# Kernel optimization log

Hardware: AMD Instinct MI355X
Metric: run time of the kernel (lower is better)

The kernel has to match this reference:

```python
import jax, jax.numpy as jnp
import numpy as np

HID = 50

def _lstm_cell(x_t, h, c, W_ih, W_hh, b_ih, b_hh):
    # PyTorch LSTMCell gate order: i, f, g, o
    gates = x_t @ W_ih.T + b_ih + h @ W_hh.T + b_hh  # [B, 4*HID]
    i, f, g, o = jnp.split(gates, 4, axis=-1)
    i = jax.nn.sigmoid(i)
    f = jax.nn.sigmoid(f)
    g = jnp.tanh(g)
    o = jax.nn.sigmoid(o)
    c = f * c + i * g
    h = o * jnp.tanh(c)
    return h, c


def setup_inputs() -> dict:
    key = jax.random.key(0)
    ks = jax.random.split(key, 8)
    B, T = 2048, 512
    stdv = 1.0 / np.sqrt(HID)
    x = jax.random.normal(ks[0], (B, T), dtype=jnp.float32)
    W_ih = jax.random.uniform(ks[1], (4 * HID, 1), jnp.float32, -stdv, stdv)
    W_hh = jax.random.uniform(ks[2], (4 * HID, HID), jnp.float32, -stdv, stdv)
    b_ih = jax.random.uniform(ks[3], (4 * HID,), jnp.float32, -stdv, stdv)
    b_hh = jax.random.uniform(ks[4], (4 * HID,), jnp.float32, -stdv, stdv)
    W_out = jax.random.uniform(ks[5], (1, HID), jnp.float32, -stdv, stdv)
    b_out = jax.random.uniform(ks[6], (1,), jnp.float32, -stdv, stdv)
    return {"x": x, "W_ih": W_ih, "W_hh": W_hh, "b_ih": b_ih,
            "b_hh": b_hh, "W_out": W_out, "b_out": b_out, "future": 64}


def reference(x, W_ih, W_hh, b_ih, b_hh, W_out, b_out, future):
    B, T = x.shape
    h0 = jnp.zeros((B, HID), dtype=x.dtype)
    c0 = jnp.zeros((B, HID), dtype=x.dtype)
    xs = x.T[:, :, None]  # [T, B, 1]

    def seq_step(carry, x_t):
        h, c = carry
        h, c = _lstm_cell(x_t, h, c, W_ih, W_hh, b_ih, b_hh)
        out = h @ W_out.T + b_out  # [B, 1]
        return (h, c), out

    (h, c), outs = jax.lax.scan(seq_step, (h0, c0), xs)  # outs: [T, B, 1]

    def fut_step(carry, _):
        h, c, out = carry
        h, c = _lstm_cell(out, h, c, W_ih, W_hh, b_ih, b_hh)
        out = h @ W_out.T + b_out
        return (h, c, out), out

    _, fut_outs = jax.lax.scan(fut_step, (h, c, outs[-1]), None, length=future)
    all_outs = jnp.concatenate([outs, fut_outs], axis=0)  # [T+future, B, 1]
    return jnp.transpose(all_outs[:, :, 0])  # [B, T+future]
```

## Files before the change

kernel.cpp:

```cpp
#include <hip/hip_runtime.h>

typedef float v2f __attribute__((ext_vector_type(2)));
typedef float v4f __attribute__((ext_vector_type(4)));

#define BATCH 2048
#define TSEQ 512
#define FUT 64
#define TOUT (TSEQ + FUT)
#define HID 50
#define RPB 4

__device__ __forceinline__ float rcp_f(float x) { return __builtin_amdgcn_rcpf(x); }
__device__ __forceinline__ float sigm(float x)  { return rcp_f(1.f + __expf(-x)); }
__device__ __forceinline__ float tanh_f(float x){ return 1.f - 2.f * rcp_f(__expf(2.f * x) + 1.f); }

__device__ __forceinline__ void pkfma(v2f& acc, v2f a, v2f b) {
  asm("v_pk_fma_f32 %0, %1, %2, %0" : "+v"(acc) : "v"(a), "v"(b));
}

__global__ __launch_bounds__(256, 2) void lstm_seq_kernel(
    const float* __restrict__ x,
    const float* __restrict__ W_ih,
    const float* __restrict__ W_hh,
    const float* __restrict__ b_ih,
    const float* __restrict__ b_hh,
    const float* __restrict__ W_out,
    const float* __restrict__ b_out,
    float* __restrict__ out)
{
  __shared__ float sW[4 * HID * HID];
  __shared__ float sx[RPB][TSEQ];
  __shared__ float sH[RPB][64];

  const int tid  = threadIdx.x;
  const int wv   = tid >> 6;
  const int lane = tid & 63;
  const int row  = blockIdx.x * RPB + wv;

  for (int i = tid; i < 4 * HID * HID; i += 256) sW[i] = W_hh[i];
  for (int i = lane; i < TSEQ; i += 64) sx[wv][i] = x[row * TSEQ + i];
  sH[wv][lane] = 0.f;
  __syncthreads();

  const bool act = (lane < HID);
  const int  kk  = act ? lane : 0;

  v2f wi[25], wf[25], wg[25], wo[25];
  {
    const v2f* r0 = (const v2f*)&sW[(0 * HID + kk) * HID];
    const v2f* r1 = (const v2f*)&sW[(1 * HID + kk) * HID];
    const v2f* r2 = (const v2f*)&sW[(2 * HID + kk) * HID];
    const v2f* r3 = (const v2f*)&sW[(3 * HID + kk) * HID];
    #pragma unroll
    for (int j = 0; j < 25; ++j) { wi[j] = r0[j]; wf[j] = r1[j]; wg[j] = r2[j]; wo[j] = r3[j]; }
  }
  const float bi = b_ih[0 * HID + kk] + b_hh[0 * HID + kk];
  const float bf = b_ih[1 * HID + kk] + b_hh[1 * HID + kk];
  const float bg = b_ih[2 * HID + kk] + b_hh[2 * HID + kk];
  const float bo = b_ih[3 * HID + kk] + b_hh[3 * HID + kk];
  const float wxi = W_ih[0 * HID + kk];
  const float wxf = W_ih[1 * HID + kk];
  const float wxg = W_ih[2 * HID + kk];
  const float wxo = W_ih[3 * HID + kk];
  const float wout = act ? W_out[kk] : 0.f;
  const float bout = b_out[0];

  float h = 0.f, c = 0.f, oprev = 0.f;
  float* orow = out + (size_t)row * TOUT;
  const v4f* sH4 = (const v4f*)sH[wv];
  const v2f* sH2 = (const v2f*)sH[wv];

  auto step = [&](float xv, int t) {
    sH[wv][lane] = h;
    v2f ai2 = {fmaf(xv, wxi, bi), 0.f};
    v2f af2 = {fmaf(xv, wxf, bf), 0.f};
    v2f ag2 = {fmaf(xv, wxg, bg), 0.f};
    v2f ao2 = {fmaf(xv, wxo, bo), 0.f};
    #pragma unroll
    for (int q = 0; q < 12; ++q) {
      v4f h4 = sH4[q];
      v2f ha = {h4.x, h4.y}, hb = {h4.z, h4.w};
      pkfma(ai2, wi[2 * q], ha); pkfma(ai2, wi[2 * q + 1], hb);
      pkfma(af2, wf[2 * q], ha); pkfma(af2, wf[2 * q + 1], hb);
      pkfma(ag2, wg[2 * q], ha); pkfma(ag2, wg[2 * q + 1], hb);
      pkfma(ao2, wo[2 * q], ha); pkfma(ao2, wo[2 * q + 1], hb);
    }
    {
      v2f ht = sH2[24];
      pkfma(ai2, wi[24], ht); pkfma(af2, wf[24], ht);
      pkfma(ag2, wg[24], ht); pkfma(ao2, wo[24], ht);
    }
    float gi = sigm(ai2.x + ai2.y);
    float gf = sigm(af2.x + af2.y);
    float gg = tanh_f(ag2.x + ag2.y);
    float go = sigm(ao2.x + ao2.y);
    c = fmaf(gf, c, gi * gg);
    float hn = go * tanh_f(c);
    h = act ? hn : 0.f;
    float p = h * wout;
    p += __shfl_xor(p, 1);
    p += __shfl_xor(p, 2);
    p += __shfl_xor(p, 4);
    p += __shfl_xor(p, 8);
    p += __shfl_xor(p, 16);
    p += __shfl_xor(p, 32);
    float ot = p + bout;
    if (lane == 0) orow[t] = ot;
    oprev = ot;
  };

  #pragma unroll 1
  for (int t = 0; t < TSEQ; ++t) step(sx[wv][t], t);
  #pragma unroll 1
  for (int t = TSEQ; t < TOUT; ++t) step(oprev, t);
}

extern "C" void kernel_launch(void* const* d_in, const int* in_sizes, int n_in,
                              void* d_out, int out_size, void* d_ws, size_t ws_size,
                              hipStream_t stream) {
  const float* x     = (const float*)d_in[0];
  const float* W_ih  = (const float*)d_in[1];
  const float* W_hh  = (const float*)d_in[2];
  const float* b_ih  = (const float*)d_in[3];
  const float* b_hh  = (const float*)d_in[4];
  const float* W_out = (const float*)d_in[5];
  const float* b_out = (const float*)d_in[6];
  float* out = (float*)d_out;

  lstm_seq_kernel<<<BATCH / RPB, 256, 0, stream>>>(
      x, W_ih, W_hh, b_ih, b_hh, W_out, b_out, out);
}
```

Baseline: 577.7 us.

## Split LSTM gates across two waves per batch row with LDS exchange

Instead of one wave computing all four gates for one batch row, each block now handles one row with two waves: wave 0 computes the i and f gates, wave 1 computes g and o. Wave 1 passes its activations through shared memory, and wave 0 updates c and h and does the output reduction. This halves the per-thread weight registers and the serial FMA chain per step, and the weights now load directly from global memory instead of being staged through shared memory. The cost is two block barriers per timestep and a serial tail where wave 1 sits idle.

New measurement: 603.2 us. 4.4% more time.

```diff
diff --git a/kernel.cpp b/kernel.cpp
--- a/kernel.cpp
+++ b/kernel.cpp
@@ -8,7 +8,7 @@
 #define FUT 64
 #define TOUT (TSEQ + FUT)
 #define HID 50
-#define RPB 4
+
 
 __device__ __forceinline__ float rcp_f(float x) { return __builtin_amdgcn_rcpf(x); }
 __device__ __forceinline__ float sigm(float x)  { return rcp_f(1.f + __expf(-x)); }
@@ -18,7 +18,7 @@
   asm("v_pk_fma_f32 %0, %1, %2, %0" : "+v"(acc) : "v"(a), "v"(b));
 }
 
-__global__ __launch_bounds__(256, 2) void lstm_seq_kernel(
+__global__ __launch_bounds__(128, 3) void lstm_seq_kernel(
     const float* __restrict__ x,
     const float* __restrict__ W_ih,
     const float* __restrict__ W_hh,
@@ -28,91 +28,85 @@
     const float* __restrict__ b_out,
     float* __restrict__ out)
 {
-  __shared__ float sW[4 * HID * HID];
-  __shared__ float sx[RPB][TSEQ];
-  __shared__ float sH[RPB][64];
+  __shared__ float sH[64];
+  __shared__ v2f   sGb[HID];
+  __shared__ float sOut[1];
+  __shared__ float sx[TSEQ];
 
   const int tid  = threadIdx.x;
   const int wv   = tid >> 6;
   const int lane = tid & 63;
-  const int row  = blockIdx.x * RPB + wv;
+  const int row  = blockIdx.x;
 
-  for (int i = tid; i < 4 * HID * HID; i += 256) sW[i] = W_hh[i];
-  for (int i = lane; i < TSEQ; i += 64) sx[wv][i] = x[row * TSEQ + i];
-  sH[wv][lane] = 0.f;
-  __syncthreads();
+  for (int i = tid; i < TSEQ; i += 128) sx[i] = x[row * TSEQ + i];
+  if (tid < 64) sH[tid] = 0.f;
 
   const bool act = (lane < HID);
   const int  kk  = act ? lane : 0;
+  const int  rA  = (2 * wv) * HID + kk;
+  const int  rB  = (2 * wv + 1) * HID + kk;
 
-  v2f wi[25], wf[25], wg[25], wo[25];
+  v2f wA[25], wB[25];
   {
-    const v2f* r0 = (const v2f*)&sW[(0 * HID + kk) * HID];
-    const v2f* r1 = (const v2f*)&sW[(1 * HID + kk) * HID];
-    const v2f* r2 = (const v2f*)&sW[(2 * HID + kk) * HID];
-    const v2f* r3 = (const v2f*)&sW[(3 * HID + kk) * HID];
+    const v2f* pA = (const v2f*)(W_hh + rA * HID);
+    const v2f* pB = (const v2f*)(W_hh + rB * HID);
     #pragma unroll
-    for (int j = 0; j < 25; ++j) { wi[j] = r0[j]; wf[j] = r1[j]; wg[j] = r2[j]; wo[j] = r3[j]; }
+    for (int j = 0; j < 25; ++j) { wA[j] = pA[j]; wB[j] = pB[j]; }
   }
-  const float bi = b_ih[0 * HID + kk] + b_hh[0 * HID + kk];
-  const float bf = b_ih[1 * HID + kk] + b_hh[1 * HID + kk];
-  const float bg = b_ih[2 * HID + kk] + b_hh[2 * HID + kk];
-  const float bo = b_ih[3 * HID + kk] + b_hh[3 * HID + kk];
-  const float wxi = W_ih[0 * HID + kk];
-  const float wxf = W_ih[1 * HID + kk];
-  const float wxg = W_ih[2 * HID + kk];
-  const float wxo = W_ih[3 * HID + kk];
+  const float bA  = b_ih[rA] + b_hh[rA];
+  const float bB  = b_ih[rB] + b_hh[rB];
+  const float wxA = W_ih[rA];
+  const float wxB = W_ih[rB];
   const float wout = act ? W_out[kk] : 0.f;
   const float bout = b_out[0];
 
-  float h = 0.f, c = 0.f, oprev = 0.f;
+  float c = 0.f;
   float* orow = out + (size_t)row * TOUT;
-  const v4f* sH4 = (const v4f*)sH[wv];
-  const v2f* sH2 = (const v2f*)sH[wv];
+  const v4f* sH4 = (const v4f*)sH;
+  const v2f* sH2 = (const v2f*)sH;
 
-  auto step = [&](float xv, int t) {
-    sH[wv][lane] = h;
-    v2f ai2 = {fmaf(xv, wxi, bi), 0.f};
-    v2f af2 = {fmaf(xv, wxf, bf), 0.f};
-    v2f ag2 = {fmaf(xv, wxg, bg), 0.f};
-    v2f ao2 = {fmaf(xv, wxo, bo), 0.f};
+  __syncthreads();
+
+  #pragma unroll 1
+  for (int t = 0; t < TOUT; ++t) {
+    const float xv = (t < TSEQ) ? sx[t] : sOut[0];
+
+    v2f aA = {fmaf(xv, wxA, bA), 0.f};
+    v2f aB = {fmaf(xv, wxB, bB), 0.f};
     #pragma unroll
     for (int q = 0; q < 12; ++q) {
       v4f h4 = sH4[q];
       v2f ha = {h4.x, h4.y}, hb = {h4.z, h4.w};
-      pkfma(ai2, wi[2 * q], ha); pkfma(ai2, wi[2 * q + 1], hb);
-      pkfma(af2, wf[2 * q], ha); pkfma(af2, wf[2 * q + 1], hb);
-      pkfma(ag2, wg[2 * q], ha); pkfma(ag2, wg[2 * q + 1], hb);
-      pkfma(ao2, wo[2 * q], ha); pkfma(ao2, wo[2 * q + 1], hb);
+      pkfma(aA, wA[2 * q], ha); pkfma(aA, wA[2 * q + 1], hb);
+      pkfma(aB, wB[2 * q], ha); pkfma(aB, wB[2 * q + 1], hb);
     }
-    {
-      v2f ht = sH2[24];
-      pkfma(ai2, wi[24], ht); pkfma(af2, wf[24], ht);
-      pkfma(ag2, wg[24], ht); pkfma(ao2, wo[24], ht);
+    { v2f ht = sH2[24]; pkfma(aA, wA[24], ht); pkfma(aB, wB[24], ht); }
+    const float pa = aA.x + aA.y;
+    const float pb = aB.x + aB.y;
+
+    v2f gp;
+    if (wv == 0) gp = (v2f){sigm(pa),  sigm(pb)};
+    else         gp = (v2f){tanh_f(pa), sigm(pb)};
+    if (wv == 1 && act) sGb[kk] = gp;
+    __syncthreads();
+
+    if (wv == 0) {
+      const v2f go = sGb[kk];
+      c = fmaf(gp.y, c, gp.x * go.x);
+      const float h = act ? go.y * tanh_f(c) : 0.f;
+      sH[lane] = h;
+      float p = h * wout;
+      p += __shfl_xor(p, 1);
+      p += __shfl_xor(p, 2);
+      p += __shfl_xor(p, 4);
+      p += __shfl_xor(p, 8);
+      p += __shfl_xor(p, 16);
+      p += __shfl_xor(p, 32);
+      const float ot = p + bout;
+      if (lane == 0) { orow[t] = ot; sOut[0] = ot; }
     }
-    float gi = sigm(ai2.x + ai2.y);
-    float gf = sigm(af2.x + af2.y);
-    float gg = tanh_f(ag2.x + ag2.y);
-    float go = sigm(ao2.x + ao2.y);
-    c = fmaf(gf, c, gi * gg);
-    float hn = go * tanh_f(c);
-    h = act ? hn : 0.f;
-    float p = h * wout;
-    p += __shfl_xor(p, 1);
-    p += __shfl_xor(p, 2);
-    p += __shfl_xor(p, 4);
-    p += __shfl_xor(p, 8);
-    p += __shfl_xor(p, 16);
-    p += __shfl_xor(p, 32);
-    float ot = p + bout;
-    if (lane == 0) orow[t] = ot;
-    oprev = ot;
-  };
-
-  #pragma unroll 1
-  for (int t = 0; t < TSEQ; ++t) step(sx[wv][t], t);
-  #pragma unroll 1
-  for (int t = TSEQ; t < TOUT; ++t) step(oprev, t);
+    __syncthreads();
+  }
 }
 
 extern "C" void kernel_launch(void* const* d_in, const int* in_sizes, int n_in,
@@ -127,6 +121,6 @@
   const float* b_out = (const float*)d_in[6];
   float* out = (float*)d_out;
 
-  lstm_seq_kernel<<<BATCH / RPB, 256, 0, stream>>>(
+  lstm_seq_kernel<<<BATCH, 128, 0, stream>>>(
       x, W_ih, W_hh, b_ih, b_hh, W_out, b_out, out);
 }
```

## Fold output projection into recurrent weights for future steps, drop LDS weight staging

Applied to the files above, without the earlier changes.

Loads W_hh rows straight from global memory into registers instead of staging the whole matrix through shared memory, which removes a 40KB LDS footprint and that copy. During the autoregressive future phase, the input x_t = W_out·h + b_out is folded algebraically into the recurrent weights and biases, so the feedback no longer has to wait on the cross-lane reduction. The two phases are merged into one loop with a one-time weight update at t == TSEQ. This changes floating-point rounding slightly and adds a branch to every iteration of the loop.

After: 584.8 us. Within noise of the previous version (+1.2%).

```diff
diff --git a/kernel.cpp b/kernel.cpp
--- a/kernel.cpp
+++ b/kernel.cpp
@@ -9,6 +9,7 @@
 #define TOUT (TSEQ + FUT)
 #define HID 50
 #define RPB 4
+
 
 __device__ __forceinline__ float rcp_f(float x) { return __builtin_amdgcn_rcpf(x); }
 __device__ __forceinline__ float sigm(float x)  { return rcp_f(1.f + __expf(-x)); }
@@ -28,7 +29,6 @@
     const float* __restrict__ b_out,
     float* __restrict__ out)
 {
-  __shared__ float sW[4 * HID * HID];
   __shared__ float sx[RPB][TSEQ];
   __shared__ float sH[RPB][64];
 
@@ -37,9 +37,9 @@
   const int lane = tid & 63;
   const int row  = blockIdx.x * RPB + wv;
 
-  for (int i = tid; i < 4 * HID * HID; i += 256) sW[i] = W_hh[i];
-  for (int i = lane; i < TSEQ; i += 64) sx[wv][i] = x[row * TSEQ + i];
-  sH[wv][lane] = 0.f;
+  for (int i = tid; i < RPB * TSEQ; i += 256)
+    ((float*)sx)[i] = x[blockIdx.x * RPB * TSEQ + i];
+  if (tid < RPB * 64) ((float*)sH)[tid] = 0.f;
   __syncthreads();
 
   const bool act = (lane < HID);
@@ -47,17 +47,17 @@
 
   v2f wi[25], wf[25], wg[25], wo[25];
   {
-    const v2f* r0 = (const v2f*)&sW[(0 * HID + kk) * HID];
-    const v2f* r1 = (const v2f*)&sW[(1 * HID + kk) * HID];
-    const v2f* r2 = (const v2f*)&sW[(2 * HID + kk) * HID];
-    const v2f* r3 = (const v2f*)&sW[(3 * HID + kk) * HID];
+    const v2f* r0 = (const v2f*)(W_hh + (0 * HID + kk) * HID);
+    const v2f* r1 = (const v2f*)(W_hh + (1 * HID + kk) * HID);
+    const v2f* r2 = (const v2f*)(W_hh + (2 * HID + kk) * HID);
+    const v2f* r3 = (const v2f*)(W_hh + (3 * HID + kk) * HID);
     #pragma unroll
     for (int j = 0; j < 25; ++j) { wi[j] = r0[j]; wf[j] = r1[j]; wg[j] = r2[j]; wo[j] = r3[j]; }
   }
-  const float bi = b_ih[0 * HID + kk] + b_hh[0 * HID + kk];
-  const float bf = b_ih[1 * HID + kk] + b_hh[1 * HID + kk];
-  const float bg = b_ih[2 * HID + kk] + b_hh[2 * HID + kk];
-  const float bo = b_ih[3 * HID + kk] + b_hh[3 * HID + kk];
+  float bi = b_ih[0 * HID + kk] + b_hh[0 * HID + kk];
+  float bf = b_ih[1 * HID + kk] + b_hh[1 * HID + kk];
+  float bg = b_ih[2 * HID + kk] + b_hh[2 * HID + kk];
+  float bo = b_ih[3 * HID + kk] + b_hh[3 * HID + kk];
   const float wxi = W_ih[0 * HID + kk];
   const float wxf = W_ih[1 * HID + kk];
   const float wxg = W_ih[2 * HID + kk];
@@ -65,38 +65,57 @@
   const float wout = act ? W_out[kk] : 0.f;
   const float bout = b_out[0];
 
-  float h = 0.f, c = 0.f, oprev = 0.f;
+  float h = 0.f, c = 0.f;
   float* orow = out + (size_t)row * TOUT;
   const v4f* sH4 = (const v4f*)sH[wv];
   const v2f* sH2 = (const v2f*)sH[wv];
 
-  auto step = [&](float xv, int t) {
+  #pragma unroll 1
+  for (int t = 0; t < TOUT; ++t) {
+    if (t == TSEQ) {
+      const v2f* wo2 = (const v2f*)W_out;
+      const v2f xi = {wxi, wxi}, xf = {wxf, wxf}, xg = {wxg, wxg}, xo = {wxo, wxo};
+      #pragma unroll
+      for (int j = 0; j < 25; ++j) {
+        const v2f wv_ = wo2[j];
+        pkfma(wi[j], xi, wv_);
+        pkfma(wf[j], xf, wv_);
+        pkfma(wg[j], xg, wv_);
+        pkfma(wo[j], xo, wv_);
+      }
+      bi = fmaf(wxi, bout, bi);
+      bf = fmaf(wxf, bout, bf);
+      bg = fmaf(wxg, bout, bg);
+      bo = fmaf(wxo, bout, bo);
+    }
+    const float xv = (t < TSEQ) ? sx[wv][t] : 0.f;
+
     sH[wv][lane] = h;
-    v2f ai2 = {fmaf(xv, wxi, bi), 0.f};
-    v2f af2 = {fmaf(xv, wxf, bf), 0.f};
-    v2f ag2 = {fmaf(xv, wxg, bg), 0.f};
-    v2f ao2 = {fmaf(xv, wxo, bo), 0.f};
+
+    v2f ai = {fmaf(xv, wxi, bi), 0.f};
+    v2f af = {fmaf(xv, wxf, bf), 0.f};
+    v2f ag = {fmaf(xv, wxg, bg), 0.f};
+    v2f ao = {fmaf(xv, wxo, bo), 0.f};
     #pragma unroll
     for (int q = 0; q < 12; ++q) {
-      v4f h4 = sH4[q];
-      v2f ha = {h4.x, h4.y}, hb = {h4.z, h4.w};
-      pkfma(ai2, wi[2 * q], ha); pkfma(ai2, wi[2 * q + 1], hb);
-      pkfma(af2, wf[2 * q], ha); pkfma(af2, wf[2 * q + 1], hb);
-      pkfma(ag2, wg[2 * q], ha); pkfma(ag2, wg[2 * q + 1], hb);
-      pkfma(ao2, wo[2 * q], ha); pkfma(ao2, wo[2 * q + 1], hb);
+      const v4f h4 = sH4[q];
+      const v2f ha = {h4.x, h4.y}, hb = {h4.z, h4.w};
+      pkfma(ai, wi[2 * q], ha); pkfma(ai, wi[2 * q + 1], hb);
+      pkfma(af, wf[2 * q], ha); pkfma(af, wf[2 * q + 1], hb);
+      pkfma(ag, wg[2 * q], ha); pkfma(ag, wg[2 * q + 1], hb);
+      pkfma(ao, wo[2 * q], ha); pkfma(ao, wo[2 * q + 1], hb);
     }
-    {
-      v2f ht = sH2[24];
-      pkfma(ai2, wi[24], ht); pkfma(af2, wf[24], ht);
-      pkfma(ag2, wg[24], ht); pkfma(ao2, wo[24], ht);
-    }
-    float gi = sigm(ai2.x + ai2.y);
-    float gf = sigm(af2.x + af2.y);
-    float gg = tanh_f(ag2.x + ag2.y);
-    float go = sigm(ao2.x + ao2.y);
+    { const v2f ht = sH2[24];
+      pkfma(ai, wi[24], ht); pkfma(af, wf[24], ht);
+      pkfma(ag, wg[24], ht); pkfma(ao, wo[24], ht); }
+
+    const float gi = sigm(ai.x + ai.y);
+    const float gf = sigm(af.x + af.y);
+    const float gg = tanh_f(ag.x + ag.y);
+    const float go = sigm(ao.x + ao.y);
     c = fmaf(gf, c, gi * gg);
-    float hn = go * tanh_f(c);
-    h = act ? hn : 0.f;
+    h = act ? go * tanh_f(c) : 0.f;
+
     float p = h * wout;
     p += __shfl_xor(p, 1);
     p += __shfl_xor(p, 2);
@@ -104,15 +123,8 @@
     p += __shfl_xor(p, 8);
     p += __shfl_xor(p, 16);
     p += __shfl_xor(p, 32);
-    float ot = p + bout;
-    if (lane == 0) orow[t] = ot;
-    oprev = ot;
-  };
-
-  #pragma unroll 1
-  for (int t = 0; t < TSEQ; ++t) step(sx[wv][t], t);
-  #pragma unroll 1
-  for (int t = TSEQ; t < TOUT; ++t) step(oprev, t);
+    if (lane == 0) orow[t] = p + bout;
+  }
 }
 
 extern "C" void kernel_launch(void* const* d_in, const int* in_sizes, int n_in,
```
